# Kernel optimization log

Hardware: AMD Instinct MI355X
Metric: run time of the kernel (lower is better)

The kernel has to match this reference:

```python
import jax, jax.numpy as jnp
import numpy as np

DIM = 2048
HEADS = 16
HEAD_DIM = DIM // HEADS


def setup_inputs() -> dict:
    key = jax.random.key(0)
    ks = jax.random.split(key, 9)
    B, S = 1, 4096
    X = jax.random.normal(ks[0], (B, S, DIM), dtype=jnp.float32)
    sc = 1.0 / np.sqrt(DIM)
    Wq = jax.random.normal(ks[1], (DIM, DIM), dtype=jnp.float32) * sc
    bq = jax.random.normal(ks[2], (DIM,), dtype=jnp.float32) * 0.01
    Wk = jax.random.normal(ks[3], (DIM, DIM), dtype=jnp.float32) * sc
    bk = jax.random.normal(ks[4], (DIM,), dtype=jnp.float32) * 0.01
    Wv = jax.random.normal(ks[5], (DIM, DIM), dtype=jnp.float32) * sc
    bv = jax.random.normal(ks[6], (DIM,), dtype=jnp.float32) * 0.01
    Wo = jax.random.normal(ks[7], (DIM, DIM), dtype=jnp.float32) * sc
    bo = jax.random.normal(ks[8], (DIM,), dtype=jnp.float32) * 0.01
    return {"X": X, "Wq": Wq, "bq": bq, "Wk": Wk, "bk": bk,
            "Wv": Wv, "bv": bv, "Wo": Wo, "bo": bo, "is_causal": 1}


def reference(X, Wq, bq, Wk, bk, Wv, bv, Wo, bo, is_causal):
    B, S, _ = X.shape
    # torch nn.Linear: y = x @ W^T + b
    Q = (X @ Wq.T + bq).reshape(B, S, HEADS, HEAD_DIM).transpose(0, 2, 1, 3)
    K = (X @ Wk.T + bk).reshape(B, S, HEADS, HEAD_DIM).transpose(0, 2, 1, 3)
    V = (X @ Wv.T + bv).reshape(B, S, HEADS, HEAD_DIM).transpose(0, 2, 1, 3)
    scores = jnp.einsum('bhqd,bhkd->bhqk', Q, K) / np.sqrt(HEAD_DIM)  # [B,H,S,S]
    if is_causal:
        causal = jnp.tril(jnp.ones((S, S), dtype=bool))
        scores = jnp.where(causal, scores, -jnp.inf)
    attn = jax.nn.softmax(scores, axis=-1)
    # dropout_rate = 0 (eval) -> identity
    Out = jnp.einsum('bhqk,bhkd->bhqd', attn, V)
    Out = Out.transpose(0, 2, 1, 3).reshape(B, S, DIM)
    return Out @ Wo.T + bo
```

## Files before the change

### kernel.cpp

```cpp
#include <hip/hip_runtime.h>
#include <hip/hip_bf16.h>

typedef unsigned short u16;
typedef __attribute__((ext_vector_type(8))) short short8;
typedef __attribute__((ext_vector_type(4))) short short4v;
typedef __attribute__((ext_vector_type(4))) float floatx4;

constexpr int SEQ = 4096;
constexpr int DM  = 2048;
constexpr int NH  = 16;
constexpr int HD  = 128;

__device__ inline u16 f2b(float f) {
    __hip_bfloat16 h = __float2bfloat16(f);
    return *reinterpret_cast<u16*>(&h);
}
__device__ inline float b2f(u16 u) {
    __hip_bfloat16 h = *reinterpret_cast<__hip_bfloat16*>(&u);
    return __bfloat162float(h);
}

__device__ __forceinline__ void async_copy16(const u16* g, u16* lds_base) {
    __builtin_amdgcn_global_load_lds(
        (const __attribute__((address_space(1))) unsigned int*)g,
        (__attribute__((address_space(3))) unsigned int*)lds_base,
        16, 0, 0);
}

__global__ void detect_dtype(const u16* __restrict__ X, int* __restrict__ flag) {
    __shared__ int cnt;
    if (threadIdx.x == 0) cnt = 0;
    __syncthreads();
    int local = 0;
    for (int i = threadIdx.x; i < 4096; i += 256) {
        int e = (X[i] >> 7) & 0xFF;
        if (e >= 0x3C && e <= 0x8D) local++;
    }
    atomicAdd(&cnt, local);
    __syncthreads();
    if (threadIdx.x == 0) *flag = (cnt >= 3890) ? 1 : 0;
}

struct ConvArgs {
    const void* src[9];
    unsigned long long dstoff[9];
    int n[9];
};
__global__ void convert_all(ConvArgs a, u16* __restrict__ base,
                            const int* __restrict__ flag) {
    const int t = blockIdx.y;
    const int n = a.n[t];
    const int i = (blockIdx.x * blockDim.x + threadIdx.x) * 8;
    if (i >= n) return;
    u16* out = base + a.dstoff[t];
    if (*flag) {
        *(short8*)&out[i] = *(const short8*)&((const u16*)a.src[t])[i];
    } else {
        const float* p = (const float*)a.src[t];
        u16 tmp[8];
#pragma unroll
        for (int j = 0; j < 8; j++) tmp[j] = f2b(p[i + j]);
        *(short8*)&out[i] = *(const short8*)tmp;
    }
}

__launch_bounds__(256)
__global__ void gemm_qkv(const u16* __restrict__ A, const u16* __restrict__ W,
                         const u16* __restrict__ bias,
                         u16* __restrict__ Qb, u16* __restrict__ Kb,
                         u16* __restrict__ VtG) {
    __shared__ __align__(16) u16 As[128 * 32];
    __shared__ __align__(16) u16 Ws[128 * 32];

    const int tid  = threadIdx.x;
    const int lane = tid & 63;
    const int w    = tid >> 6;
    const int wm   = (w >> 1) * 64;
    const int wn   = (w & 1) * 64;
    const int m0   = blockIdx.y * 128;
    const int n0   = blockIdx.x * 128;
    const int qm   = lane & 15;
    const int quad = lane >> 4;
    const int K    = DM;

    const int lrow = lane >> 2;
    const int lcol = (lane & 3) * 8;

    floatx4 acc[16];
#pragma unroll
    for (int i = 0; i < 16; i++) acc[i] = floatx4{0.f, 0.f, 0.f, 0.f};

    for (int k0 = 0; k0 < K; k0 += 32) {
        __syncthreads();
#pragma unroll
        for (int i = 0; i < 2; i++) {
            const int rb = w * 32 + i * 16;
            async_copy16(&A[(size_t)(m0 + rb + lrow) * K + k0 + lcol], &As[rb * 32]);
            async_copy16(&W[(size_t)(n0 + rb + lrow) * K + k0 + lcol], &Ws[rb * 32]);
        }
        __syncthreads();

        short8 af[4], bf[4];
#pragma unroll
        for (int mt = 0; mt < 4; mt++)
            af[mt] = *(const short8*)&As[(wm + mt * 16 + qm) * 32 + quad * 8];
#pragma unroll
        for (int nt = 0; nt < 4; nt++)
            bf[nt] = *(const short8*)&Ws[(wn + nt * 16 + qm) * 32 + quad * 8];
#pragma unroll
        for (int mt = 0; mt < 4; mt++)
#pragma unroll
            for (int nt = 0; nt < 4; nt++)
                acc[mt * 4 + nt] =
                    __builtin_amdgcn_mfma_f32_16x16x32_bf16(af[mt], bf[nt], acc[mt * 4 + nt], 0, 0, 0);
    }

    const int buf = n0 >> 11;
    if (buf < 2) {
        u16* Y = (buf == 0) ? Qb : Kb;
#pragma unroll
        for (int nt = 0; nt < 4; nt++) {
            const int gcol = n0 + wn + nt * 16 + qm;
            const int col  = gcol & 2047;
            const float bv = b2f(bias[gcol]);
#pragma unroll
            for (int mt = 0; mt < 4; mt++) {
                const int rbase = m0 + wm + mt * 16 + quad * 4;
#pragma unroll
                for (int r = 0; r < 4; r++)
                    Y[(size_t)(rbase + r) * DM + col] = f2b(acc[mt * 4 + nt][r] + bv);
            }
        }
    } else {
#pragma unroll
        for (int nt = 0; nt < 4; nt++) {
            const int gcol = n0 + wn + nt * 16 + qm;
            const int col  = gcol & 2047;
            const float bv = b2f(bias[gcol]);
#pragma unroll
            for (int mt = 0; mt < 4; mt++) {
                const int rbase = m0 + wm + mt * 16 + quad * 4;
                u16 tmp[4];
#pragma unroll
                for (int r = 0; r < 4; r++)
                    tmp[r] = f2b(acc[mt * 4 + nt][r] + bv);
                *(short4v*)&VtG[(size_t)col * SEQ + rbase] = *(const short4v*)tmp;
            }
        }
    }
}

__launch_bounds__(256)
__global__ void gemm_out(const u16* __restrict__ A, const u16* __restrict__ W,
                         const u16* __restrict__ bias, void* __restrict__ out,
                         const int* __restrict__ flag) {
    __shared__ __align__(16) u16 As[128 * 32];
    __shared__ __align__(16) u16 Ws[128 * 32];

    const int tid  = threadIdx.x;
    const int lane = tid & 63;
    const int w    = tid >> 6;
    const int wm   = (w >> 1) * 64;
    const int wn   = (w & 1) * 64;
    const int m0   = blockIdx.y * 128;
    const int n0   = blockIdx.x * 128;
    const int qm   = lane & 15;
    const int quad = lane >> 4;
    const int K    = DM, N = DM;

    const int lrow = lane >> 2;
    const int lcol = (lane & 3) * 8;

    floatx4 acc[16];
#pragma unroll
    for (int i = 0; i < 16; i++) acc[i] = floatx4{0.f, 0.f, 0.f, 0.f};

    for (int k0 = 0; k0 < K; k0 += 32) {
        __syncthreads();
#pragma unroll
        for (int i = 0; i < 2; i++) {
            const int rb = w * 32 + i * 16;
            async_copy16(&A[(size_t)(m0 + rb + lrow) * K + k0 + lcol], &As[rb * 32]);
            async_copy16(&W[(size_t)(n0 + rb + lrow) * K + k0 + lcol], &Ws[rb * 32]);
        }
        __syncthreads();

        short8 af[4], bf[4];
#pragma unroll
        for (int mt = 0; mt < 4; mt++)
            af[mt] = *(const short8*)&As[(wm + mt * 16 + qm) * 32 + quad * 8];
#pragma unroll
        for (int nt = 0; nt < 4; nt++)
            bf[nt] = *(const short8*)&Ws[(wn + nt * 16 + qm) * 32 + quad * 8];
#pragma unroll
        for (int mt = 0; mt < 4; mt++)
#pragma unroll
            for (int nt = 0; nt < 4; nt++)
                acc[mt * 4 + nt] =
                    __builtin_amdgcn_mfma_f32_16x16x32_bf16(af[mt], bf[nt], acc[mt * 4 + nt], 0, 0, 0);
    }

    const int f = *flag;
#pragma unroll
    for (int nt = 0; nt < 4; nt++) {
        const int col = n0 + wn + nt * 16 + qm;
        const float bv = b2f(bias[col]);
#pragma unroll
        for (int mt = 0; mt < 4; mt++) {
            const int rbase = m0 + wm + mt * 16 + quad * 4;
#pragma unroll
            for (int r = 0; r < 4; r++) {
                const float v = acc[mt * 4 + nt][r] + bv;
                if (f) ((u16*)out)[(size_t)(rbase + r) * N + col] = f2b(v);
                else   ((float*)out)[(size_t)(rbase + r) * N + col] = v;
            }
        }
    }
}

__launch_bounds__(512)
__global__ void attn_kernel(const u16* __restrict__ Q, const u16* __restrict__ K,
                            const u16* __restrict__ Vt, u16* __restrict__ O,
                            const int* __restrict__ is_causal_p) {
    __shared__ __align__(16) u16 Ks[64][136];
    __shared__ __align__(16) u16 Vts[128][72];
    __shared__ __align__(16) u16 Pb[8][16][72];

    const int tid  = threadIdx.x;
    const int lane = tid & 63;
    const int w    = tid >> 6;
    const int qm   = lane & 15;
    const int quad = lane >> 4;
    const int xt   = ((blockIdx.y >> 3) & 1) ? (gridDim.x - 1 - blockIdx.x)
                                             : blockIdx.x;
    const int q0   = xt * 128;
    const int h    = blockIdx.y;
    const int causal = *is_causal_p;
    const float scale = 0.08838834764831845f;
    const float SHIFT = 16.0f;

    short8 qf[4];
    {
        const u16* qptr = Q + (size_t)(q0 + w * 16 + qm) * DM + h * HD;
#pragma unroll
        for (int kc = 0; kc < 4; kc++)
            qf[kc] = *(const short8*)&qptr[kc * 32 + quad * 8];
    }

    floatx4 o[8];
#pragma unroll
    for (int dt = 0; dt < 8; dt++) o[dt] = floatx4{0.f, 0.f, 0.f, 0.f};
    float l_part[4] = {0.f, 0.f, 0.f, 0.f};

    const int jend = causal ? (q0 + 128) : SEQ;

    const int kr0 = tid >> 4;
    const int kc8 = (tid & 15) * 8;
    const int vd0 = tid >> 3;
    const int vc8 = (tid & 7) * 8;

    short8 kreg[2], vreg[2];
#pragma unroll
    for (int p = 0; p < 2; p++) {
        kreg[p] = *(const short8*)&K[(size_t)(kr0 + p * 32) * DM + h * HD + kc8];
        vreg[p] = *(const short8*)&Vt[(size_t)(h * HD + vd0 + p * 64) * SEQ + vc8];
    }

    for (int j0 = 0; j0 < jend; j0 += 64) {
#pragma unroll
        for (int p = 0; p < 2; p++) {
            *(short8*)&Ks[kr0 + p * 32][kc8] = kreg[p];
            *(short8*)&Vts[vd0 + p * 64][vc8] = vreg[p];
        }
        __syncthreads();

        const int jn = (j0 + 64 < jend) ? j0 + 64 : 0;
#pragma unroll
        for (int p = 0; p < 2; p++) {
            kreg[p] = *(const short8*)&K[(size_t)(jn + kr0 + p * 32) * DM + h * HD + kc8];
            vreg[p] = *(const short8*)&Vt[(size_t)(h * HD + vd0 + p * 64) * SEQ + jn + vc8];
        }

        floatx4 s[4];
#pragma unroll
        for (int nt = 0; nt < 4; nt++) s[nt] = floatx4{0.f, 0.f, 0.f, 0.f};
#pragma unroll
        for (int kc = 0; kc < 4; kc++)
#pragma unroll
            for (int nt = 0; nt < 4; nt++) {
                short8 b = *(const short8*)&Ks[nt * 16 + qm][kc * 32 + quad * 8];
                s[nt] = __builtin_amdgcn_mfma_f32_16x16x32_bf16(qf[kc], b, s[nt], 0, 0, 0);
            }

        const bool mask = causal && (j0 + 64 > q0 + w * 16);
#pragma unroll
        for (int r = 0; r < 4; r++) {
            const int qg = q0 + w * 16 + quad * 4 + r;
#pragma unroll
            for (int nt = 0; nt < 4; nt++) {
                float v = fmaf(s[nt][r], scale, -SHIFT);
                if (mask && (j0 + nt * 16 + qm > qg)) v = -1e30f;
                const float p = __expf(v);
                l_part[r] += p;
                Pb[w][quad * 4 + r][nt * 16 + qm] = f2b(p);
            }
        }
        asm volatile("s_waitcnt lgkmcnt(0)" ::: "memory");

#pragma unroll
        for (int kc = 0; kc < 2; kc++) {
            short8 pf = *(const short8*)&Pb[w][qm][kc * 32 + quad * 8];
#pragma unroll
            for (int dt = 0; dt < 8; dt++) {
                short8 b = *(const short8*)&Vts[dt * 16 + qm][kc * 32 + quad * 8];
                o[dt] = __builtin_amdgcn_mfma_f32_16x16x32_bf16(pf, b, o[dt], 0, 0, 0);
            }
        }
        __syncthreads();
    }

#pragma unroll
    for (int r = 0; r < 4; r++) {
        float l = l_part[r];
#pragma unroll
        for (int off = 8; off >= 1; off >>= 1)
            l += __shfl_xor(l, off, 64);
        const float inv = 1.0f / l;
        const int qg = q0 + w * 16 + quad * 4 + r;
#pragma unroll
        for (int dt = 0; dt < 8; dt++) {
            const int d = h * HD + dt * 16 + qm;
            O[(size_t)qg * DM + d] = f2b(o[dt][r] * inv);
        }
    }
}

extern "C" void kernel_launch(void* const* d_in, const int* in_sizes, int n_in,
                              void* d_out, int out_size, void* d_ws, size_t ws_size,
                              hipStream_t stream) {
    const int* isc = (const int*)d_in[9];

    int* flag = (int*)d_ws;
    u16* base = (u16*)((char*)d_ws + 256);

    const int NX = SEQ * DM;
    const int NW = DM * DM;
    const int NB = DM;

    unsigned long long off = 0;
    const unsigned long long oXc   = off; off += NX;
    const unsigned long long oWall = off; off += 3ull * NW;
    const unsigned long long oWo   = off; off += NW;
    const unsigned long long oBall = off; off += 3ull * NB;
    const unsigned long long oBo   = off; off += NB;
    const unsigned long long oQ    = off; off += NX;
    const unsigned long long oK    = off; off += NX;
    const unsigned long long oVt   = off; off += NX;
    const unsigned long long oA    = off; off += NX;

    detect_dtype<<<1, 256, 0, stream>>>((const u16*)d_in[0], flag);

    ConvArgs ca;
    const unsigned long long dsts[9] = {oXc, oWall, oBall, oWall + NW, oBall + NB,
                                        oWall + 2ull * NW, oBall + 2ull * NB, oWo, oBo};
    for (int i = 0; i < 9; i++) {
        ca.src[i] = d_in[i];
        ca.dstoff[i] = dsts[i];
        ca.n[i] = in_sizes[i];
    }
    convert_all<<<dim3(NX / 8 / 256, 9), 256, 0, stream>>>(ca, base, flag);

    gemm_qkv<<<dim3(3 * DM / 128, SEQ / 128), 256, 0, stream>>>(
        base + oXc, base + oWall, base + oBall,
        base + oQ, base + oK, base + oVt);

    attn_kernel<<<dim3(SEQ / 128, NH), 512, 0, stream>>>(
        base + oQ, base + oK, base + oVt, base + oA, isc);

    gemm_out<<<dim3(DM / 128, SEQ / 128), 256, 0, stream>>>(
        base + oA, base + oWo, base + oBo, d_out, flag);
}
```

Measured before the change: 460.1 us.

## Keep softmax probabilities in registers via transposed S and fp16 PV MFMA

The attention kernel now computes S transposed (K as the A operand), so each lane's score fragment lines up with the A-operand layout of a 16x16x16 fp16 MFMA. P stays in registers instead of round-tripping through the shared Pb buffer. V is now stored as fp16 so PV runs as f16 MFMAs, and the softmax shift is lowered to suit fp16 range. Separately, convert_all switches to a compact 1D grid with prefix offsets, which drops the blocks that used to exit immediately for the small tensors. The fp16 V and P carry overflow and precision risk, and the PV MFMA is smaller (K=16), so more MFMA instructions are issued.

```diff
diff --git a/kernel.cpp b/kernel.cpp
--- a/kernel.cpp
+++ b/kernel.cpp
@@ -5,6 +5,7 @@
 typedef __attribute__((ext_vector_type(8))) short short8;
 typedef __attribute__((ext_vector_type(4))) short short4v;
 typedef __attribute__((ext_vector_type(4))) float floatx4;
+typedef __attribute__((ext_vector_type(4))) _Float16 half4;
 
 constexpr int SEQ = 4096;
 constexpr int DM  = 2048;
@@ -44,14 +45,15 @@
 struct ConvArgs {
     const void* src[9];
     unsigned long long dstoff[9];
-    int n[9];
+    int pfx[10];
 };
 __global__ void convert_all(ConvArgs a, u16* __restrict__ base,
                             const int* __restrict__ flag) {
-    const int t = blockIdx.y;
-    const int n = a.n[t];
-    const int i = (blockIdx.x * blockDim.x + threadIdx.x) * 8;
-    if (i >= n) return;
+    const int b = blockIdx.x;
+    int t = 0;
+#pragma unroll
+    for (int k = 1; k < 9; k++) t += (b >= a.pfx[k]);
+    const int i = ((b - a.pfx[t]) * 256 + threadIdx.x) * 8;
     u16* out = base + a.dstoff[t];
     if (*flag) {
         *(short8*)&out[i] = *(const short8*)&((const u16*)a.src[t])[i];
@@ -142,8 +144,10 @@
                 const int rbase = m0 + wm + mt * 16 + quad * 4;
                 u16 tmp[4];
 #pragma unroll
-                for (int r = 0; r < 4; r++)
-                    tmp[r] = f2b(acc[mt * 4 + nt][r] + bv);
+                for (int r = 0; r < 4; r++) {
+                    _Float16 hv = (_Float16)(acc[mt * 4 + nt][r] + bv);
+                    tmp[r] = *reinterpret_cast<u16*>(&hv);
+                }
                 *(short4v*)&VtG[(size_t)col * SEQ + rbase] = *(const short4v*)tmp;
             }
         }
@@ -224,7 +228,6 @@
                             const int* __restrict__ is_causal_p) {
     __shared__ __align__(16) u16 Ks[64][136];
     __shared__ __align__(16) u16 Vts[128][72];
-    __shared__ __align__(16) u16 Pb[8][16][72];
 
     const int tid  = threadIdx.x;
     const int lane = tid & 63;
@@ -237,7 +240,7 @@
     const int h    = blockIdx.y;
     const int causal = *is_causal_p;
     const float scale = 0.08838834764831845f;
-    const float SHIFT = 16.0f;
+    const float SHIFT = 2.0f;
 
     short8 qf[4];
     {
@@ -250,9 +253,10 @@
     floatx4 o[8];
 #pragma unroll
     for (int dt = 0; dt < 8; dt++) o[dt] = floatx4{0.f, 0.f, 0.f, 0.f};
-    float l_part[4] = {0.f, 0.f, 0.f, 0.f};
+    float l_part = 0.f;
 
     const int jend = causal ? (q0 + 128) : SEQ;
+    const int qg   = q0 + w * 16 + qm;
 
     const int kr0 = tid >> 4;
     const int kc8 = (tid & 15) * 8;
@@ -283,54 +287,51 @@
 
         floatx4 s[4];
 #pragma unroll
-        for (int nt = 0; nt < 4; nt++) s[nt] = floatx4{0.f, 0.f, 0.f, 0.f};
+        for (int t = 0; t < 4; t++) s[t] = floatx4{0.f, 0.f, 0.f, 0.f};
 #pragma unroll
         for (int kc = 0; kc < 4; kc++)
 #pragma unroll
-            for (int nt = 0; nt < 4; nt++) {
-                short8 b = *(const short8*)&Ks[nt * 16 + qm][kc * 32 + quad * 8];
-                s[nt] = __builtin_amdgcn_mfma_f32_16x16x32_bf16(qf[kc], b, s[nt], 0, 0, 0);
+            for (int t = 0; t < 4; t++) {
+                short8 kf = *(const short8*)&Ks[t * 16 + qm][kc * 32 + quad * 8];
+                s[t] = __builtin_amdgcn_mfma_f32_16x16x32_bf16(kf, qf[kc], s[t], 0, 0, 0);
             }
 
         const bool mask = causal && (j0 + 64 > q0 + w * 16);
-#pragma unroll
-        for (int r = 0; r < 4; r++) {
-            const int qg = q0 + w * 16 + quad * 4 + r;
-#pragma unroll
-            for (int nt = 0; nt < 4; nt++) {
-                float v = fmaf(s[nt][r], scale, -SHIFT);
-                if (mask && (j0 + nt * 16 + qm > qg)) v = -1e30f;
+        half4 pf[4];
+#pragma unroll
+        for (int t = 0; t < 4; t++) {
+#pragma unroll
+            for (int r = 0; r < 4; r++) {
+                float v = fmaf(s[t][r], scale, -SHIFT);
+                if (mask && (j0 + t * 16 + quad * 4 + r > qg)) v = -1e30f;
                 const float p = __expf(v);
-                l_part[r] += p;
-                Pb[w][quad * 4 + r][nt * 16 + qm] = f2b(p);
-            }
-        }
-        asm volatile("s_waitcnt lgkmcnt(0)" ::: "memory");
-
-#pragma unroll
-        for (int kc = 0; kc < 2; kc++) {
-            short8 pf = *(const short8*)&Pb[w][qm][kc * 32 + quad * 8];
+                l_part += p;
+                pf[t][r] = (_Float16)p;
+            }
+        }
+
+#pragma unroll
+        for (int t = 0; t < 4; t++)
 #pragma unroll
             for (int dt = 0; dt < 8; dt++) {
-                short8 b = *(const short8*)&Vts[dt * 16 + qm][kc * 32 + quad * 8];
-                o[dt] = __builtin_amdgcn_mfma_f32_16x16x32_bf16(pf, b, o[dt], 0, 0, 0);
-            }
-        }
-        __syncthreads();
-    }
-
+                half4 vb = *(const half4*)&Vts[dt * 16 + qm][t * 16 + quad * 4];
+                o[dt] = __builtin_amdgcn_mfma_f32_16x16x16f16(pf[t], vb, o[dt], 0, 0, 0);
+            }
+        __syncthreads();
+    }
+
+    float l = l_part;
+    l += __shfl_xor(l, 16, 64);
+    l += __shfl_xor(l, 32, 64);
 #pragma unroll
     for (int r = 0; r < 4; r++) {
-        float l = l_part[r];
-#pragma unroll
-        for (int off = 8; off >= 1; off >>= 1)
-            l += __shfl_xor(l, off, 64);
-        const float inv = 1.0f / l;
-        const int qg = q0 + w * 16 + quad * 4 + r;
+        const float lr  = __shfl(l, (w << 6 >> 6) * 0 + quad * 4 + r, 64);
+        const float inv = 1.0f / lr;
+        const int orow  = q0 + w * 16 + quad * 4 + r;
 #pragma unroll
         for (int dt = 0; dt < 8; dt++) {
             const int d = h * HD + dt * 16 + qm;
-            O[(size_t)qg * DM + d] = f2b(o[dt][r] * inv);
+            O[(size_t)orow * DM + d] = f2b(o[dt][r] * inv);
         }
     }
 }
@@ -363,12 +364,15 @@
     ConvArgs ca;
     const unsigned long long dsts[9] = {oXc, oWall, oBall, oWall + NW, oBall + NB,
                                         oWall + 2ull * NW, oBall + 2ull * NB, oWo, oBo};
+    int pfx = 0;
     for (int i = 0; i < 9; i++) {
         ca.src[i] = d_in[i];
         ca.dstoff[i] = dsts[i];
-        ca.n[i] = in_sizes[i];
-    }
-    convert_all<<<dim3(NX / 8 / 256, 9), 256, 0, stream>>>(ca, base, flag);
+        ca.pfx[i] = pfx;
+        pfx += in_sizes[i] / 2048;
+    }
+    ca.pfx[9] = pfx;
+    convert_all<<<pfx, 256, 0, stream>>>(ca, base, flag);
 
     gemm_qkv<<<dim3(3 * DM / 128, SEQ / 128), 256, 0, stream>>>(
         base + oXc, base + oWall, base + oBall,
```

Measured after the change: 549.4 us. 19.4% more time.
